# Kernel tuning notes

Hardware: AMD Instinct MI355X
Metric: run time of the kernel (lower is better)

## Reference

```python
import jax, jax.numpy as jnp
import numpy as np
from jax import lax

IMG_SIZE = 608
STRIDE = 32
NUM_CLASSES = 20
CONF_THRESH = 0.001
NMS_THRESH = 0.6
SLOPE = 0.1
B = 16
P5 = 512
FMP = IMG_SIZE // STRIDE   # 19
N = FMP * FMP              # 361 boxes per image


def _conv(x, w, b):
    y = lax.conv_general_dilated(x, w, (1, 1), 'SAME',
                                 dimension_numbers=('NCHW', 'OIHW', 'NCHW'))
    return y + b[None, :, None, None]


def _conv_act(x, w, b):
    # Conv block (conv + folded-BN bias + LeakyReLU(0.1)) at inference
    return jax.nn.leaky_relu(_conv(x, w, b), SLOPE)


def _grid():
    gy, gx = jnp.meshgrid(jnp.arange(FMP), jnp.arange(FMP), indexing='ij')
    return jnp.stack([gx, gy], axis=-1).reshape(-1, 2).astype(jnp.float32)  # [N,2]


def _decode(reg):
    # reg: [B,N,4] raw head output -> normalized x1y1x2y2 clamped to [0,1]
    xy = jax.nn.sigmoid(reg[..., :2]) + _grid()[None]          # center_sample=False
    wh = jnp.exp(reg[..., 2:])
    box = jnp.concatenate([xy - wh * 0.5, xy + wh * 0.5], axis=-1)
    return jnp.clip(box * (STRIDE / IMG_SIZE), 0.0, 1.0)


def _nms_one_class(boxes, s):
    # boxes: [N,4]; s: [N] scores with -1 marking boxes not of this class / below conf
    order = jnp.argsort(-s)
    b = boxes[order]
    valid = s[order] >= CONF_THRESH
    x1, y1, x2, y2 = b[:, 0], b[:, 1], b[:, 2], b[:, 3]
    areas = (x2 - x1) * (y2 - y1)
    w = jnp.maximum(1e-28, jnp.minimum(x2[:, None], x2[None, :]) - jnp.maximum(x1[:, None], x1[None, :]))
    h = jnp.maximum(1e-28, jnp.minimum(y2[:, None], y2[None, :]) - jnp.maximum(y1[:, None], y1[None, :]))
    inter = w * h
    iou = inter / (areas[:, None] + areas[None, :] - inter + 1e-14)  # [N,N]
    later = jnp.arange(N)[None, :] > jnp.arange(N)[:, None]
    sup = (iou > NMS_THRESH) & later

    def body(i, keep):
        # box i suppresses later boxes only if itself still kept (greedy NMS)
        return keep & ~(sup[i] & keep[i])

    keep = lax.fori_loop(0, N, body, valid)
    return jnp.zeros(N, dtype=bool).at[order].set(keep)  # back to original order


def _postprocess(boxes, scores):
    # per image: boxes [N,4], scores [N,C]
    cls_inds = jnp.argmax(scores, axis=-1)
    sc = jnp.max(scores, axis=-1)
    cmask = (cls_inds[None, :] == jnp.arange(NUM_CLASSES)[:, None]) & (sc >= CONF_THRESH)[None, :]
    masked = jnp.where(cmask, sc[None, :], -1.0)  # [C,N]
    keep_c = jax.vmap(_nms_one_class, in_axes=(None, 0))(boxes, masked)
    return sc, cls_inds, jnp.any(keep_c, axis=0)


def setup_inputs() -> dict:
    key = jax.random.key(0)
    ks = jax.random.split(key, 16)
    inp = {'x': jax.random.normal(ks[0], (B, P5, FMP, FMP), jnp.float32)}
    names = ['cls1', 'cls2', 'reg1', 'reg2', 'reg3', 'reg4']
    for j, nm in enumerate(names):
        inp['w_' + nm] = jax.random.normal(ks[1 + j], (P5, P5, 3, 3), jnp.float32) * 0.02
        inp['b_' + nm] = jnp.zeros((P5,), jnp.float32)
    inp['w_obj'] = jax.random.normal(ks[8], (1, P5, 1, 1), jnp.float32) * 0.01
    inp['b_obj'] = jnp.zeros((1,), jnp.float32)
    inp['w_clsh'] = jax.random.normal(ks[9], (NUM_CLASSES, P5, 1, 1), jnp.float32) * 0.01
    inp['b_clsh'] = jnp.zeros((NUM_CLASSES,), jnp.float32)
    inp['w_regh'] = jax.random.normal(ks[10], (4, P5, 1, 1), jnp.float32) * 0.01
    inp['b_regh'] = jnp.zeros((4,), jnp.float32)
    return inp


def reference(x, w_cls1, b_cls1, w_cls2, b_cls2, w_reg1, b_reg1, w_reg2, b_reg2,
              w_reg3, b_reg3, w_reg4, b_reg4, w_obj, b_obj, w_clsh, b_clsh,
              w_regh, b_regh):
    cf = _conv_act(_conv_act(x, w_cls1, b_cls1), w_cls2, b_cls2)
    rf = x
    for wv, bv in ((w_reg1, b_reg1), (w_reg2, b_reg2), (w_reg3, b_reg3), (w_reg4, b_reg4)):
        rf = _conv_act(rf, wv, bv)

    def flat(t):  # [B,C,H,W] -> [B,N,C]
        return t.reshape(t.shape[0], t.shape[1], -1).transpose(0, 2, 1)

    obj = flat(_conv(rf, w_obj, b_obj))      # [B,N,1]
    clsp = flat(_conv(cf, w_clsh, b_clsh))   # [B,N,C]
    regp = flat(_conv(rf, w_regh, b_regh))   # [B,N,4]

    boxes = _decode(regp)                                        # [B,N,4]
    scores = jax.nn.sigmoid(obj) * jax.nn.softmax(clsp, axis=-1)  # [B,N,C]
    sc, cls_inds, keep = jax.vmap(_postprocess)(boxes, scores)
    # fixed-shape outputs: boxes [B,N,4], per-box best score [B,N],
    # class index [B,N], NMS keep mask [B,N]
    return boxes, sc, cls_inds, keep
```

## Files before the change

### kernel.cpp

```cpp
#include <hip/hip_runtime.h>
#include <hip/hip_bf16.h>
#include <stdint.h>

typedef __bf16 bf16x8 __attribute__((ext_vector_type(8)));
typedef float  f32x16 __attribute__((ext_vector_type(16)));

#define FMPX 19
#define NPOS 361
#define CCH  512
#define NB   16
#define NCLS 20
#define CONF_T 0.001f
#define NMS_TH 0.6f
#define BSCALE (32.0f/608.0f)

#define SC_OFF   (NB*NPOS*4)
#define CLS_OFF  (SC_OFF + NB*NPOS)
#define KEEP_OFF (CLS_OFF + NB*NPOS)

#define GSTR  3528
#define PLANE ((size_t)3612672)
#define WSL   294912
#define XBUF  16384
#define WBUF  18432
#define WOFF  32768
#define SMEMB 69632

__device__ __forceinline__ void gl_lds16(const void* g, void* l) {
  __builtin_amdgcn_global_load_lds(
      (const __attribute__((address_space(1))) unsigned int*)g,
      (__attribute__((address_space(3))) unsigned int*)l, 16, 0, 0);
}
#define MFMA32(A,B,C) __builtin_amdgcn_mfma_f32_32x32x16_bf16(A,B,C,0,0,0)
#define SBAR() __builtin_amdgcn_sched_barrier(0)
#define PRIO1 __builtin_amdgcn_s_setprio(1)
#define PRIO0 __builtin_amdgcn_s_setprio(0)

__global__ void split_x_k(const float* __restrict__ x, __bf16* __restrict__ Xd) {
  __shared__ float sx[8][368];
  int g = blockIdx.x, b = blockIdx.y;
  int tid = threadIdx.x;
  for (int i = tid; i < 8*361; i += 256) {
    int ci = i / 361, p = i - ci*361;
    sx[ci][p] = x[((size_t)b*CCH + g*8 + ci)*NPOS + p];
  }
  __syncthreads();
  for (int row = tid; row < 441; row += 256) {
    int y = row/21, xx = row - y*21;
    bf16x8 oh = {}, om = {};
    if (y >= 1 && y <= 19 && xx >= 1 && xx <= 19) {
      int p = (y-1)*19 + xx - 1;
#pragma unroll
      for (int j = 0; j < 8; ++j) {
        float v = sx[j][p];
        __bf16 hh = (__bf16)v;
        oh[j] = hh; om[j] = (__bf16)(v - (float)hh);
      }
    }
    size_t o = (((size_t)b)*64 + g)*GSTR + (size_t)row*8;
    *(bf16x8*)(Xd + o)         = oh;
    *(bf16x8*)(Xd + PLANE + o) = om;
  }
}

__global__ void repack_k(const float* __restrict__ w, __bf16* __restrict__ Wg) {
  __shared__ float sw[32][145];
  int slice = blockIdx.x, chunk = blockIdx.y;
  int tid = threadIdx.x;
  for (int i = tid; i < 32*144; i += 256) {
    int cl = i / 144, r = i - cl*144;
    sw[cl][r] = w[((size_t)slice*32 + cl)*4608 + chunk*144 + r];
  }
  __syncthreads();
  for (int u = tid; u < 1152; u += 256) {
    int co = u & 31, kh = (u >> 5) & 1, pt = u >> 6;
    int tap = pt % 9, pl = pt / 9;
    bf16x8 o;
#pragma unroll
    for (int j = 0; j < 8; ++j) {
      float v = sw[co][(kh*8 + j)*9 + tap];
      __bf16 hh = (__bf16)v;
      o[j] = pl == 0 ? hh : (__bf16)(v - (float)hh);
    }
    *(bf16x8*)(Wg + (((size_t)(slice*2 + pl)*9 + tap)*32 + chunk)*512 + kh*256 + co*8) = o;
  }
}

#define RD6X(SP, AT, IMM) do { \
  SP##0 = *(const bf16x8*)(Xc + AT##0 + (IMM)); \
  SP##1 = *(const bf16x8*)(Xc + AT##1 + (IMM)); \
  SP##2 = *(const bf16x8*)(Xc + AT##2 + (IMM)); \
  SP##3 = *(const bf16x8*)(Xc + AT##3 + (IMM)); \
  SP##4 = *(const bf16x8*)(Xc + AT##4 + (IMM)); \
  SP##5 = *(const bf16x8*)(Xc + AT##5 + (IMM)); } while (0)

#define CL(SP, BH_, BM_) do { PRIO1; \
  acc0 = MFMA32(SP##0, BH_, acc0); acc1 = MFMA32(SP##1, BH_, acc1); \
  acc2 = MFMA32(SP##2, BH_, acc2); acc3 = MFMA32(SP##3, BH_, acc3); \
  acc4 = MFMA32(SP##4, BH_, acc4); acc5 = MFMA32(SP##5, BH_, acc5); \
  acc0 = MFMA32(SP##0, BM_, acc0); acc1 = MFMA32(SP##1, BM_, acc1); \
  acc2 = MFMA32(SP##2, BM_, acc2); acc3 = MFMA32(SP##3, BM_, acc3); \
  acc4 = MFMA32(SP##4, BM_, acc4); acc5 = MFMA32(SP##5, BM_, acc5); \
  PRIO0; } while (0)

#define CLH(SP, B_) do { PRIO1; \
  acc0 = MFMA32(SP##0, B_, acc0); acc1 = MFMA32(SP##1, B_, acc1); \
  acc2 = MFMA32(SP##2, B_, acc2); acc3 = MFMA32(SP##3, B_, acc3); \
  acc4 = MFMA32(SP##4, B_, acc4); acc5 = MFMA32(SP##5, B_, acc5); \
  PRIO0; } while (0)

#define STO(A, MTL) do { _Pragma("unroll") \
  for (int r = 0; r < 16; ++r) { \
    Lf[wq*3456 + ((MTL)*32 + 4*kh + (r & 3) + 8*(r >> 2))*36 + col] = (A)[r]; } } while (0)

__global__ __launch_bounds__(256, 2) void conv3x3_mfma(
    const __bf16* __restrict__ Xs, const __bf16* __restrict__ Wg,
    const float* __restrict__ bias, __bf16* __restrict__ Xd)
{
  __shared__ __attribute__((aligned(16))) char smem[SMEMB];
  const int tid = threadIdx.x;
  const int bid = blockIdx.x;
  const int b = bid & 15, slice = (bid >> 4) & 15, h = bid >> 8;
  const int lane = tid & 63;
  const int wq = __builtin_amdgcn_readfirstlane(tid >> 6);
  const int col = lane & 31, kh = lane >> 5;
  const int kh4096 = kh*4096;
  const int PB = h*190, CNT = h ? 171 : 190;
  const int PEND = PB + CNT - 1;
  const int clampU = h ? 230 : 251;

  int ab0, ab1, ab2, ab3, ab4, ab5;
  {
    int ao[6];
#pragma unroll
    for (int mt = 0; mt < 6; ++mt) {
      int p = PB + mt*32 + col; if (p > PEND) p = PEND;
      int pp = p + 2*(p/19) + 22;
      ao[mt] = (pp - h*210)*16;
    }
    ab0 = ao[0]; ab1 = ao[1]; ab2 = ao[2]; ab3 = ao[3]; ab4 = ao[4]; ab5 = ao[5];
  }
  const int boff = kh*512 + col*16;

  const int goffs[9] = {-352,-336,-320,-16,0,16,320,336,352};
  const int t0 = 2*wq, t1 = t0 + 1;
  const int g0 = goffs[t0], g1 = goffs[t1];
  const int a8im = 352 + ((wq & 2) ? 8192 : 0);
  const int t0a0 = ab0+g0, t0a1 = ab1+g0, t0a2 = ab2+g0,
            t0a3 = ab3+g0, t0a4 = ab4+g0, t0a5 = ab5+g0;
  const int t1a0 = ab0+g1, t1a1 = ab1+g1, t1a2 = ab2+g1,
            t1a3 = ab3+g1, t1a4 = ab4+g1, t1a5 = ab5+g1;
  const int t8a0 = ab0+a8im, t8a1 = ab1+a8im, t8a2 = ab2+a8im,
            t8a3 = ab3+a8im, t8a4 = ab4+a8im, t8a5 = ab5+a8im;
  const int wb0 = t0*1024 + boff, wb1 = t1*1024 + boff;
  const int wb8 = 8192 + boff + ((wq & 1) ? 9216 : 0);

  int ux = wq*64 + lane; if (ux > clampU) ux = clampU;
  const __bf16* xsb = Xs + (size_t)b*64*GSTR + (size_t)(h*210 + ux)*8;
  const __bf16* wsb = Wg + (size_t)slice*WSL + (size_t)lane*8;
  int wsrc0, wsrc1, wsrc2, wsrc3, wsrc4;
  int wdst0, wdst1, wdst2, wdst3, wdst4;
  {
    int ws[5], wd[5];
#pragma unroll
    for (int q = 0; q < 5; ++q) {
      int wk = wq*5 + q; if (wk > 17) wk = 17;
      int pl = wk > 8 ? 1 : 0, tap = wk - 9*pl;
      ws[q] = ((pl*9 + tap)*32)*512;
      wd[q] = WOFF + pl*9216 + tap*1024;
    }
    wsrc0 = ws[0]; wsrc1 = ws[1]; wsrc2 = ws[2]; wsrc3 = ws[3]; wsrc4 = ws[4];
    wdst0 = wd[0]; wdst1 = wd[1]; wdst2 = wd[2]; wdst3 = wd[3]; wdst4 = wd[4];
  }
  const bool wv3 = (wq*5 + 3) < 18, wv4 = (wq*5 + 4) < 18;

  auto stage = [&](int c1, int buf) {
    const __bf16* xs = xsb + (size_t)(2*c1)*GSTR;
    char* xd = smem + (buf ? XBUF : 0) + wq*1024;
    gl_lds16(xs,                    xd);
    gl_lds16(xs + GSTR,             xd + 4096);
    gl_lds16(xs + PLANE,            xd + 8192);
    gl_lds16(xs + PLANE + GSTR,     xd + 12288);
    const __bf16* wsc = wsb + (size_t)c1*512;
    char* wb = smem + (buf ? WBUF : 0);
    gl_lds16(wsc + wsrc0, wb + wdst0);
    gl_lds16(wsc + wsrc1, wb + wdst1);
    gl_lds16(wsc + wsrc2, wb + wdst2);
    if (wv3) gl_lds16(wsc + wsrc3, wb + wdst3);
    if (wv4) gl_lds16(wsc + wsrc4, wb + wdst4);
  };

  f32x16 acc0 = {}, acc1 = {}, acc2 = {}, acc3 = {}, acc4 = {}, acc5 = {};

  stage(0, 0);
  __syncthreads();

  for (int c = 0; c < 32; ++c) {
    const char* Xc = smem + (c & 1)*XBUF + kh4096;
    const char* Wc = smem + WOFF + (c & 1)*WBUF;
    if (c < 31) stage(c + 1, (c + 1) & 1);

    bf16x8 H0, H1, H2, H3, H4, H5;
    bf16x8 M0, M1, M2, M3, M4, M5;
    bf16x8 N0, N1, N2, N3, N4, N5;
    bf16x8 B0h, B0m, B1h, B1m, B8;

    RD6X(H, t0a, 0);
    B0h = *(const bf16x8*)(Wc + wb0);
    B0m = *(const bf16x8*)(Wc + wb0 + 9216);
    SBAR();
    RD6X(M, t0a, 8192);
    RD6X(N, t1a, 0);
    B1h = *(const bf16x8*)(Wc + wb1);
    B1m = *(const bf16x8*)(Wc + wb1 + 9216);
    SBAR();
    CL(H, B0h, B0m);
    SBAR();
    CL(M, B0h, B0m);
    SBAR();
    RD6X(M, t1a, 8192);
    RD6X(H, t8a, 0);
    B8 = *(const bf16x8*)(Wc + wb8);
    SBAR();
    CL(N, B1h, B1m);
    SBAR();
    CL(M, B1h, B1m);
    SBAR();
    CLH(H, B8);
    __syncthreads();
  }

  float* Lf = (float*)smem;
#pragma unroll
  for (int half = 0; half < 2; ++half) {
    if (half == 0) { STO(acc0, 0); STO(acc1, 1); STO(acc2, 2); }
    else           { STO(acc3, 0); STO(acc4, 1); STO(acc5, 2); }
    __syncthreads();
    for (int u = tid; u < 768; u += 256) {
      int pl = u / 384, rem = u - pl*384;
      int gq = rem / 96, lp = rem - gq*96;
      int lpos = half*96 + lp;
      if (lpos < CNT) {
        int p = PB + lpos;
        int pp = p + 2*(p/19) + 22;
        const float* bb = bias + slice*32 + gq*8;
        bf16x8 o;
#pragma unroll
        for (int j = 0; j < 8; ++j) {
          int coix = lp*36 + gq*8 + j;
          float v = Lf[coix] + Lf[3456 + coix] + Lf[6912 + coix] + Lf[10368 + coix] + bb[j];
          v = v > 0.f ? v : 0.1f*v;
          __bf16 hh = (__bf16)v;
          o[j] = pl == 0 ? hh : (__bf16)(v - (float)hh);
        }
        *(bf16x8*)(Xd + (((size_t)pl*16 + b)*64 + slice*4 + gq)*GSTR + (size_t)pp*8) = o;
      }
    }
    __syncthreads();
  }

  const int nh = h ? 39 : 41;
  for (int u = tid; u < 8*nh; u += 256) {
    int pl = u / (4*nh); int rem = u - pl*4*nh;
    int gq = rem / nh; int ci2 = rem - gq*nh;
    int rowpos;
    if (ci2 < 21) rowpos = h ? (420 + ci2) : ci2;
    else { int q = ci2 - 21; rowpos = ((h ? 11 : 1) + (q >> 1))*21 + 20*(q & 1); }
    bf16x8 z = {};
    *(bf16x8*)(Xd + (((size_t)pl*16 + b)*64 + slice*4 + gq)*GSTR + (size_t)rowpos*8) = z;
  }
}

__global__ __launch_bounds__(256) void head_rf_k(
    const __bf16* __restrict__ F, const float* __restrict__ wobj,
    const float* __restrict__ bobj, const float* __restrict__ wreg,
    const float* __restrict__ breg, float* __restrict__ obj, float* __restrict__ regp)
{
  int gw = blockIdx.x*4 + (threadIdx.x >> 6);
  if (gw >= NB*NPOS) return;
  int lane = threadIdx.x & 63;
  int b = gw / NPOS, p = gw % NPOS;
  int pp = p + 2*(p/19) + 22;
  const __bf16* base = F + (((size_t)b)*64 + lane)*GSTR + (size_t)pp*8;
  bf16x8 v0 = *(const bf16x8*)base;
  bf16x8 v1 = *(const bf16x8*)(base + PLANE);
  float f[8];
#pragma unroll
  for (int j = 0; j < 8; ++j) f[j] = (float)v0[j] + (float)v1[j];
#pragma unroll
  for (int o = 0; o < 5; ++o) {
    const float* wp = (o == 0) ? wobj : wreg + (o-1)*CCH;
    float4 wa = *(const float4*)(wp + lane*8);
    float4 wb = *(const float4*)(wp + lane*8 + 4);
    float s2 = f[0]*wa.x + f[1]*wa.y + f[2]*wa.z + f[3]*wa.w
             + f[4]*wb.x + f[5]*wb.y + f[6]*wb.z + f[7]*wb.w;
#pragma unroll
    for (int d = 32; d; d >>= 1) s2 += __shfl_xor(s2, d);
    if (lane == 0) {
      if (o == 0) obj[gw] = s2 + bobj[0];
      else regp[(size_t)gw*4 + (o-1)] = s2 + breg[o-1];
    }
  }
}

__global__ __launch_bounds__(256) void head_cls_k(
    const __bf16* __restrict__ F, const float* __restrict__ wcls,
    const float* __restrict__ bcls, float* __restrict__ clsp)
{
  int gw = blockIdx.x*4 + (threadIdx.x >> 6);
  if (gw >= NB*NPOS) return;
  int lane = threadIdx.x & 63;
  int b = gw / NPOS, p = gw % NPOS;
  int pp = p + 2*(p/19) + 22;
  const __bf16* base = F + (((size_t)b)*64 + lane)*GSTR + (size_t)pp*8;
  bf16x8 v0 = *(const bf16x8*)base;
  bf16x8 v1 = *(const bf16x8*)(base + PLANE);
  float f[8];
#pragma unroll
  for (int j = 0; j < 8; ++j) f[j] = (float)v0[j] + (float)v1[j];
#pragma unroll
  for (int o = 0; o < NCLS; ++o) {
    const float* wp = wcls + o*CCH;
    float4 wa = *(const float4*)(wp + lane*8);
    float4 wb = *(const float4*)(wp + lane*8 + 4);
    float s2 = f[0]*wa.x + f[1]*wa.y + f[2]*wa.z + f[3]*wa.w
             + f[4]*wb.x + f[5]*wb.y + f[6]*wb.z + f[7]*wb.w;
#pragma unroll
    for (int d = 32; d; d >>= 1) s2 += __shfl_xor(s2, d);
    if (lane == 0) clsp[(size_t)gw*NCLS + o] = s2 + bcls[o];
  }
}

__global__ void decode_k(const float* __restrict__ obj, const float* __restrict__ clsp,
                         const float* __restrict__ regp, float* __restrict__ outb)
{
  int i = blockIdx.x * 256 + threadIdx.x;
  if (i >= NB * NPOS) return;
  int p = i % NPOS;
  float gx = (float)(p % FMPX), gy = (float)(p / FMPX);
  float4 rg = *(const float4*)&regp[(size_t)i * 4];
  float cx = 1.f / (1.f + expf(-rg.x)) + gx;
  float cy = 1.f / (1.f + expf(-rg.y)) + gy;
  float whw = expf(rg.z), whh = expf(rg.w);
  float x1 = fminf(fmaxf((cx - whw * 0.5f) * BSCALE, 0.f), 1.f);
  float y1 = fminf(fmaxf((cy - whh * 0.5f) * BSCALE, 0.f), 1.f);
  float x2 = fminf(fmaxf((cx + whw * 0.5f) * BSCALE, 0.f), 1.f);
  float y2 = fminf(fmaxf((cy + whh * 0.5f) * BSCALE, 0.f), 1.f);
  outb[(size_t)i * 4 + 0] = x1; outb[(size_t)i * 4 + 1] = y1;
  outb[(size_t)i * 4 + 2] = x2; outb[(size_t)i * 4 + 3] = y2;

  float so = 1.f / (1.f + expf(-obj[i]));
  float cv[20];
  const float4* cp = (const float4*)&clsp[(size_t)i * 20];
#pragma unroll
  for (int q = 0; q < 5; q++) {
    float4 v4 = cp[q];
    cv[q * 4] = v4.x; cv[q * 4 + 1] = v4.y; cv[q * 4 + 2] = v4.z; cv[q * 4 + 3] = v4.w;
  }
  float mx = cv[0];
#pragma unroll
  for (int c = 1; c < 20; c++) mx = fmaxf(mx, cv[c]);
  float sum = 0.f;
#pragma unroll
  for (int c = 0; c < 20; c++) { cv[c] = expf(cv[c] - mx); sum += cv[c]; }
  float inv = so / sum;
  float best = -1.f; int bi = 0;
#pragma unroll
  for (int c = 0; c < 20; c++) { float s = cv[c] * inv; if (s > best) { best = s; bi = c; } }
  outb[SC_OFF + i] = best;
  outb[CLS_OFF + i] = (float)bi;
  outb[KEEP_OFF + i] = 0.f;
}

__device__ inline unsigned ordf(float f) {
  unsigned u = __float_as_uint(f);
  return (u & 0x80000000u) ? ~u : (u | 0x80000000u);
}

__global__ __launch_bounds__(64) void nms_k(const float* __restrict__ outb, float* __restrict__ keep_out)
{
  int b = blockIdx.x / NCLS, c = blockIdx.x % NCLS;
  int lane = threadIdx.x;
  __shared__ unsigned long long keys[512];
  __shared__ float bx1[384], by1[384], bx2[384], by2[384], bar[384];
  __shared__ unsigned kp[384];
  __shared__ int sj[384];

  for (int i = lane; i < 512; i += 64) {
    unsigned long long key = 0ULL;
    if (i < NPOS) {
      float sc = outb[SC_OFF + b * NPOS + i];
      int ci = (int)outb[CLS_OFF + b * NPOS + i];
      float s = (ci == c && sc >= CONF_T) ? sc : -1.0f;
      key = ((unsigned long long)ordf(s) << 32) | (unsigned)(~(unsigned)i);
    }
    keys[i] = key;
  }
  __syncthreads();
  for (int kk = 2; kk <= 512; kk <<= 1) {
    for (int jj = kk >> 1; jj > 0; jj >>= 1) {
      for (int i = lane; i < 512; i += 64) {
        int l2 = i ^ jj;
        if (l2 > i) {
          unsigned long long a = keys[i], bb2 = keys[l2];
          bool dir = (i & kk) == 0;
          bool sw = dir ? (a < bb2) : (a > bb2);
          if (sw) { keys[i] = bb2; keys[l2] = a; }
        }
      }
      __syncthreads();
    }
  }
  unsigned ordc = ordf(CONF_T);
  int nvalid = 0;
  for (int i = lane; i < 384; i += 64) {
    unsigned long long key = keys[i];
    unsigned hi = (unsigned)(key >> 32);
    int j = (int)(~(unsigned)key);
    bool valid = (key != 0ULL) && (hi >= ordc);
    kp[i] = valid ? 1u : 0u;
    if (valid) {
      const float* bp = &outb[(size_t)(b * NPOS + j) * 4];
      float x1 = bp[0], y1 = bp[1], x2 = bp[2], y2 = bp[3];
      bx1[i] = x1; by1[i] = y1; bx2[i] = x2; by2[i] = y2;
      bar[i] = (x2 - x1) * (y2 - y1);
      sj[i] = j;
    } else { bx1[i] = 0; by1[i] = 0; bx2[i] = 0; by2[i] = 0; bar[i] = 0; sj[i] = 0; }
    nvalid += __popcll(__ballot(valid));
  }
  __syncthreads();
  for (int i = 0; i < nvalid; ++i) {
    if (kp[i]) {
      float x1i = bx1[i], y1i = by1[i], x2i = bx2[i], y2i = by2[i], ai = bar[i];
      for (int j2 = i + 1 + lane; j2 < nvalid; j2 += 64) {
        if (kp[j2]) {
          float ww = fmaxf(1e-28f, fminf(x2i, bx2[j2]) - fmaxf(x1i, bx1[j2]));
          float hh = fmaxf(1e-28f, fminf(y2i, by2[j2]) - fmaxf(y1i, by1[j2]));
          float inter = ww * hh;
          float iou = inter / (ai + bar[j2] - inter + 1e-14f);
          if (iou > NMS_TH) kp[j2] = 0u;
        }
      }
    }
    __syncthreads();
  }
  for (int i = lane; i < 384; i += 64)
    if (kp[i]) keep_out[b * NPOS + sj[i]] = 1.0f;
}

extern "C" void kernel_launch(void* const* d_in, const int* in_sizes, int n_in,
                              void* d_out, int out_size, void* d_ws, size_t ws_size,
                              hipStream_t stream)
{
  const float* x      = (const float*)d_in[0];
  const float* w_cls1 = (const float*)d_in[1];  const float* b_cls1 = (const float*)d_in[2];
  const float* w_cls2 = (const float*)d_in[3];  const float* b_cls2 = (const float*)d_in[4];
  const float* w_reg1 = (const float*)d_in[5];  const float* b_reg1 = (const float*)d_in[6];
  const float* w_reg2 = (const float*)d_in[7];  const float* b_reg2 = (const float*)d_in[8];
  const float* w_reg3 = (const float*)d_in[9];  const float* b_reg3 = (const float*)d_in[10];
  const float* w_reg4 = (const float*)d_in[11]; const float* b_reg4 = (const float*)d_in[12];
  const float* w_obj  = (const float*)d_in[13]; const float* b_obj  = (const float*)d_in[14];
  const float* w_clsh = (const float*)d_in[15]; const float* b_clsh = (const float*)d_in[16];
  const float* w_regh = (const float*)d_in[17]; const float* b_regh = (const float*)d_in[18];
  float* outb = (float*)d_out;

  __bf16* XsA = (__bf16*)d_ws;
  __bf16* XsB = XsA + 2*PLANE;
  __bf16* Wg  = XsB + 2*PLANE;
  float* obj  = (float*)(Wg + (size_t)16*WSL);
  float* regp = obj + NB*NPOS;
  float* clsp = regp + (size_t)NB*NPOS*4;

  auto conv = [&](const float* wsrc, const float* bsrc, const __bf16* src, __bf16* dst) {
    repack_k<<<dim3(16, 32), 256, 0, stream>>>(wsrc, Wg);
    conv3x3_mfma<<<512, 256, 0, stream>>>(src, Wg, bsrc, dst);
  };

  split_x_k<<<dim3(64, NB), 256, 0, stream>>>(x, XsA);
  conv(w_reg1, b_reg1, XsA, XsB);
  conv(w_reg2, b_reg2, XsB, XsA);
  conv(w_reg3, b_reg3, XsA, XsB);
  conv(w_reg4, b_reg4, XsB, XsA);
  head_rf_k<<<1444, 256, 0, stream>>>(XsA, w_obj, b_obj, w_regh, b_regh, obj, regp);
  split_x_k<<<dim3(64, NB), 256, 0, stream>>>(x, XsB);
  conv(w_cls1, b_cls1, XsB, XsA);
  conv(w_cls2, b_cls2, XsA, XsB);
  head_cls_k<<<1444, 256, 0, stream>>>(XsB, w_clsh, b_clsh, clsp);
  decode_k<<<(NB * NPOS + 255) / 256, 256, 0, stream>>>(obj, clsp, regp, outb);
  nms_k<<<NB * NCLS, 64, 0, stream>>>(outb, outb + KEEP_OFF);
}
```

Baseline: 727.3 us.

## Interleave LDS reads with MFMAs via sched_group_barrier and unconditional staging

Replaces the coarse sched_barrier phases with a fine-grained sched_group_barrier schedule that interleaves ds_read instructions between MFMA groups. It also reduces register pressure by reusing two A-fragment sets in a rotating pattern. The global-to-LDS staging is moved after the first fragment reads and made unconditional: the last iteration re-stages chunk 31, and waves past the 18 weight tiles reload a duplicate via the modulo. This removes branches but adds redundant loads, and the setprio window now spans the whole compute section.

```diff
diff --git a/kernel.cpp b/kernel.cpp
--- a/kernel.cpp
+++ b/kernel.cpp
@@ -32,7 +32,7 @@
       (__attribute__((address_space(3))) unsigned int*)l, 16, 0, 0);
 }
 #define MFMA32(A,B,C) __builtin_amdgcn_mfma_f32_32x32x16_bf16(A,B,C,0,0,0)
-#define SBAR() __builtin_amdgcn_sched_barrier(0)
+#define SG(m,n) __builtin_amdgcn_sched_group_barrier(m, n, 0)
 #define PRIO1 __builtin_amdgcn_s_setprio(1)
 #define PRIO0 __builtin_amdgcn_s_setprio(0)
 
@@ -94,20 +94,18 @@
   SP##4 = *(const bf16x8*)(Xc + AT##4 + (IMM)); \
   SP##5 = *(const bf16x8*)(Xc + AT##5 + (IMM)); } while (0)
 
-#define CL(SP, BH_, BM_) do { PRIO1; \
+#define CL(SP, BH_, BM_) do { \
   acc0 = MFMA32(SP##0, BH_, acc0); acc1 = MFMA32(SP##1, BH_, acc1); \
   acc2 = MFMA32(SP##2, BH_, acc2); acc3 = MFMA32(SP##3, BH_, acc3); \
   acc4 = MFMA32(SP##4, BH_, acc4); acc5 = MFMA32(SP##5, BH_, acc5); \
   acc0 = MFMA32(SP##0, BM_, acc0); acc1 = MFMA32(SP##1, BM_, acc1); \
   acc2 = MFMA32(SP##2, BM_, acc2); acc3 = MFMA32(SP##3, BM_, acc3); \
-  acc4 = MFMA32(SP##4, BM_, acc4); acc5 = MFMA32(SP##5, BM_, acc5); \
-  PRIO0; } while (0)
-
-#define CLH(SP, B_) do { PRIO1; \
+  acc4 = MFMA32(SP##4, BM_, acc4); acc5 = MFMA32(SP##5, BM_, acc5); } while (0)
+
+#define CLH(SP, B_) do { \
   acc0 = MFMA32(SP##0, B_, acc0); acc1 = MFMA32(SP##1, B_, acc1); \
   acc2 = MFMA32(SP##2, B_, acc2); acc3 = MFMA32(SP##3, B_, acc3); \
-  acc4 = MFMA32(SP##4, B_, acc4); acc5 = MFMA32(SP##5, B_, acc5); \
-  PRIO0; } while (0)
+  acc4 = MFMA32(SP##4, B_, acc4); acc5 = MFMA32(SP##5, B_, acc5); } while (0)
 
 #define STO(A, MTL) do { _Pragma("unroll") \
   for (int r = 0; r < 16; ++r) { \
@@ -164,7 +162,7 @@
     int ws[5], wd[5];
 #pragma unroll
     for (int q = 0; q < 5; ++q) {
-      int wk = wq*5 + q; if (wk > 17) wk = 17;
+      int wk = (wq*5 + q) % 18;
       int pl = wk > 8 ? 1 : 0, tap = wk - 9*pl;
       ws[q] = ((pl*9 + tap)*32)*512;
       wd[q] = WOFF + pl*9216 + tap*1024;
@@ -172,7 +170,6 @@
     wsrc0 = ws[0]; wsrc1 = ws[1]; wsrc2 = ws[2]; wsrc3 = ws[3]; wsrc4 = ws[4];
     wdst0 = wd[0]; wdst1 = wd[1]; wdst2 = wd[2]; wdst3 = wd[3]; wdst4 = wd[4];
   }
-  const bool wv3 = (wq*5 + 3) < 18, wv4 = (wq*5 + 4) < 18;
 
   auto stage = [&](int c1, int buf) {
     const __bf16* xs = xsb + (size_t)(2*c1)*GSTR;
@@ -186,8 +183,8 @@
     gl_lds16(wsc + wsrc0, wb + wdst0);
     gl_lds16(wsc + wsrc1, wb + wdst1);
     gl_lds16(wsc + wsrc2, wb + wdst2);
-    if (wv3) gl_lds16(wsc + wsrc3, wb + wdst3);
-    if (wv4) gl_lds16(wsc + wsrc4, wb + wdst4);
+    gl_lds16(wsc + wsrc3, wb + wdst3);
+    gl_lds16(wsc + wsrc4, wb + wdst4);
   };
 
   f32x16 acc0 = {}, acc1 = {}, acc2 = {}, acc3 = {}, acc4 = {}, acc5 = {};
@@ -198,35 +195,42 @@
   for (int c = 0; c < 32; ++c) {
     const char* Xc = smem + (c & 1)*XBUF + kh4096;
     const char* Wc = smem + WOFF + (c & 1)*WBUF;
-    if (c < 31) stage(c + 1, (c + 1) & 1);
-
-    bf16x8 H0, H1, H2, H3, H4, H5;
-    bf16x8 M0, M1, M2, M3, M4, M5;
-    bf16x8 N0, N1, N2, N3, N4, N5;
-    bf16x8 B0h, B0m, B1h, B1m, B8;
-
-    RD6X(H, t0a, 0);
+    const int cn = (c < 31) ? (c + 1) : 31;
+
+    bf16x8 A00, A01, A02, A03, A04, A05;
+    bf16x8 A10, A11, A12, A13, A14, A15;
+    bf16x8 B0h, B0m, B1h, B1m, B8v;
+
+    RD6X(A0, t0a, 0);
     B0h = *(const bf16x8*)(Wc + wb0);
     B0m = *(const bf16x8*)(Wc + wb0 + 9216);
-    SBAR();
-    RD6X(M, t0a, 8192);
-    RD6X(N, t1a, 0);
+    stage(cn, (c + 1) & 1);
+    PRIO1;
+    RD6X(A1, t0a, 8192);
+    CL(A0, B0h, B0m);
+    RD6X(A0, t1a, 0);
     B1h = *(const bf16x8*)(Wc + wb1);
     B1m = *(const bf16x8*)(Wc + wb1 + 9216);
-    SBAR();
-    CL(H, B0h, B0m);
-    SBAR();
-    CL(M, B0h, B0m);
-    SBAR();
-    RD6X(M, t1a, 8192);
-    RD6X(H, t8a, 0);
-    B8 = *(const bf16x8*)(Wc + wb8);
-    SBAR();
-    CL(N, B1h, B1m);
-    SBAR();
-    CL(M, B1h, B1m);
-    SBAR();
-    CLH(H, B8);
+    CL(A1, B0h, B0m);
+    RD6X(A1, t1a, 8192);
+    CL(A0, B1h, B1m);
+    RD6X(A0, t8a, 0);
+    B8v = *(const bf16x8*)(Wc + wb8);
+    CL(A1, B1h, B1m);
+    CLH(A0, B8v);
+    PRIO0;
+
+    SG(0x100, 8);
+    SG(0x70, 9);
+#pragma unroll
+    for (int i = 0; i < 6; ++i) { SG(8, 2); SG(0x100, 1); }
+#pragma unroll
+    for (int i = 0; i < 4; ++i) { SG(8, 3); SG(0x100, 2); }
+#pragma unroll
+    for (int i = 0; i < 6; ++i) { SG(8, 2); SG(0x100, 1); }
+#pragma unroll
+    for (int i = 0; i < 7; ++i) { SG(8, 1); SG(0x100, 1); }
+    SG(8, 11);
     __syncthreads();
   }
 
```

Measured after the change: 680.4 us. 1.07x faster.
